# Kernel tuning notes

Measured on AMD Instinct MI355X. Metric: run time of the kernel, lower is better.

The kernel has to match this reference:

```python
import jax, jax.numpy as jnp
import numpy as np

N_NODES = 50000
N_EDGES = 800000
IN_DIM = 128
HID = 128
OUT_DIM = 64
NUM_GRAPHS = 512
GM_P = 2.0
EPS = 1e-6


def setup_inputs() -> dict:
    key = jax.random.key(0)
    ks = jax.random.split(key, 12)
    x = jax.random.normal(ks[0], (N_NODES, IN_DIM), dtype=jnp.float32)
    edge_index = jax.random.randint(ks[1], (2, N_EDGES), 0, N_NODES, dtype=jnp.int64)
    batch = jnp.sort(jax.random.randint(ks[2], (N_NODES,), 0, NUM_GRAPHS, dtype=jnp.int64))
    def lin(k, fan_in, fan_out):
        w = jax.random.normal(k, (fan_in, fan_out), dtype=jnp.float32) / np.sqrt(fan_in)
        return w
    return {
        "x": x,
        "edge_index": edge_index,
        "batch": batch,
        # 3 GCN conv layers (weight + bias each)
        "W0": lin(ks[3], IN_DIM, HID), "b0": jnp.zeros((HID,), jnp.float32),
        "W1": lin(ks[4], HID, HID),    "b1": jnp.zeros((HID,), jnp.float32),
        "W2": lin(ks[5], HID, HID),    "b2": jnp.zeros((HID,), jnp.float32),
        # 2 FF layers: [HID->HID], [HID->OUT_DIM]
        "Wf0": lin(ks[6], HID, HID),   "bf0": jnp.zeros((HID,), jnp.float32),
        "Wf1": lin(ks[7], HID, OUT_DIM), "bf1": jnp.zeros((OUT_DIM,), jnp.float32),
    }


def _gcn_layer(h, src, dst, deg_inv_sqrt, W, b):
    # PyG GCNConv: h' = D^-1/2 (A + I) D^-1/2 (h W) + b, deg includes self-loop
    h = h @ W                                           # [N, F]
    norm = deg_inv_sqrt[src] * deg_inv_sqrt[dst]        # [E]
    msg = h[src] * norm[:, None]                        # gather + scale, [E, F]
    agg = jax.ops.segment_sum(msg, dst, num_segments=N_NODES)
    agg = agg + h * (deg_inv_sqrt * deg_inv_sqrt)[:, None]   # self-loop term (norm = 1/deg)
    return agg + b


def _gm_pool(x, batch, p):
    # sign-preserving generalized mean pool via scatter_mean
    xt = jnp.sign(x) * (jnp.abs(x) + EPS) ** p
    sums = jax.ops.segment_sum(xt, batch, num_segments=NUM_GRAPHS)
    cnt = jax.ops.segment_sum(jnp.ones((x.shape[0],), x.dtype), batch, num_segments=NUM_GRAPHS)
    pooled = sums / jnp.maximum(cnt, 1.0)[:, None]
    return jnp.sign(pooled) * (jnp.abs(pooled) + EPS) ** (1.0 / p)


def reference(x, edge_index, batch, W0, b0, W1, b1, W2, b2, Wf0, bf0, Wf1, bf1):
    src, dst = edge_index[0], edge_index[1]
    # degree of aggregation targets, with +1 for self-loops (computed once; graph is static)
    deg = jax.ops.segment_sum(jnp.ones((N_EDGES,), x.dtype), dst, num_segments=N_NODES) + 1.0
    deg_inv_sqrt = jax.lax.rsqrt(deg)

    h = _gcn_layer(x, src, dst, deg_inv_sqrt, W0, b0)
    h = jax.nn.relu(h)
    h = _gcn_layer(h, src, dst, deg_inv_sqrt, W1, b1)
    h = jax.nn.relu(h)
    h = _gcn_layer(h, src, dst, deg_inv_sqrt, W2, b2)  # no relu after last conv

    graph_repr = _gm_pool(h, batch, GM_P)              # [G, HID]
    graph_repr = jax.nn.relu(graph_repr)

    z = jax.nn.relu(graph_repr @ Wf0 + bf0)
    logits = z @ Wf1 + bf1                             # [G, OUT_DIM]
    return logits
```

## Files before the change

### kernel.cpp

```cpp
#include <hip/hip_runtime.h>

#define N_NODES   50000
#define M_PAD     50048
#define N_TILES   1564
#define GEMM_GRID 782
#define N_EDGES   800000
#define HID       128
#define OUT_DIM   64
#define NUM_GRAPHS 512
#define EPS       1e-6f
#define NBUCK     196
#define BUCKCAP   6144
#define ABLOCKS   98

typedef __attribute__((ext_vector_type(8))) short short8;
typedef __attribute__((ext_vector_type(16))) float f32x16;

static __device__ __forceinline__ unsigned short f2bf(float f) {
    unsigned u = __builtin_bit_cast(unsigned, f);
    u += 0x7FFFu + ((u >> 16) & 1u);
    return (unsigned short)(u >> 16);
}
static __device__ __forceinline__ float bf2f(unsigned short h) {
    unsigned u = ((unsigned)h) << 16;
    return __builtin_bit_cast(float, u);
}
static __device__ __forceinline__ float lo16(unsigned w) {
    return __builtin_bit_cast(float, w << 16);
}
static __device__ __forceinline__ float hi16(unsigned w) {
    return __builtin_bit_cast(float, w & 0xFFFF0000u);
}

static __device__ __forceinline__ float signpow(float x, bool sqrt_mode) {
    if (x == 0.0f) return 0.0f;
    float a = fabsf(x) + EPS;
    float v = sqrt_mode ? sqrtf(a) : a * a;
    return x > 0.0f ? v : -v;
}

__global__ void k_wsplit3(const float* __restrict__ W0, const float* __restrict__ W1,
                          const float* __restrict__ W2, short* __restrict__ Wth,
                          short* __restrict__ Wtl, int* __restrict__ gcnt) {
    int which = blockIdx.y;
    if (which == 0 && blockIdx.x == 0 && threadIdx.x < NBUCK)
        gcnt[threadIdx.x] = 0;
    const float* W = which == 0 ? W0 : (which == 1 ? W1 : W2);
    int tid = blockIdx.x * blockDim.x + threadIdx.x;
    int k = tid & 127, n = tid >> 7;
    float w = W[k * HID + n];
    unsigned short h = f2bf(w);
    Wth[which * HID * HID + n * HID + k] = (short)h;
    Wtl[which * HID * HID + n * HID + k] = (short)f2bf(w - bf2f(h));
}

__global__ __launch_bounds__(256) void k_bucketize(const int* __restrict__ ei,
                                                   int* __restrict__ gcnt,
                                                   unsigned* __restrict__ ebuf) {
    __shared__ int lcnt[NBUCK];
    __shared__ int lbase[NBUCK];
    int tid = threadIdx.x;
    for (int i = tid; i < NBUCK; i += 256) lcnt[i] = 0;
    __syncthreads();

    const uint4* src4 = (const uint4*)ei;
    const uint4* dst4 = (const uint4*)(ei + N_EDGES);
    int base4 = blockIdx.x * 2048;

    #pragma unroll 1
    for (int it = 0; it < 8; it++) {
        int i4 = base4 + it * 256 + tid;
        if (i4 < N_EDGES / 4) {
            uint4 d = dst4[i4];
            atomicAdd(&lcnt[d.x >> 8], 1);
            atomicAdd(&lcnt[d.y >> 8], 1);
            atomicAdd(&lcnt[d.z >> 8], 1);
            atomicAdd(&lcnt[d.w >> 8], 1);
        }
    }
    __syncthreads();
    for (int i = tid; i < NBUCK; i += 256) {
        lbase[i] = atomicAdd(&gcnt[i], lcnt[i]);
        lcnt[i] = 0;
    }
    __syncthreads();

    #pragma unroll 1
    for (int it = 0; it < 8; it++) {
        int i4 = base4 + it * 256 + tid;
        if (i4 < N_EDGES / 4) {
            uint4 d = dst4[i4];
            uint4 s = src4[i4];
            unsigned dd[4] = {d.x, d.y, d.z, d.w};
            unsigned ss[4] = {s.x, s.y, s.z, s.w};
            #pragma unroll
            for (int k = 0; k < 4; k++) {
                int b = dd[k] >> 8;
                int p = atomicAdd(&lcnt[b], 1);
                ebuf[(size_t)b * BUCKCAP + lbase[b] + p] = ss[k] | (dd[k] << 16);
            }
        }
    }
}

__global__ __launch_bounds__(256) void k_csr(const unsigned* __restrict__ ebuf,
                                             const int* __restrict__ gcnt,
                                             int* __restrict__ offs,
                                             float* __restrict__ dis,
                                             int* __restrict__ csr) {
    __shared__ int cntA[256];
    __shared__ int scanA[256];
    __shared__ int sbase;
    int b = blockIdx.x;
    int t = threadIdx.x;
    int n0 = b * 256;

    int v = (t < NBUCK) ? gcnt[t] : 0;
    scanA[t] = v;
    __syncthreads();
    for (int off = 1; off < 256; off <<= 1) {
        int u = (t >= off) ? scanA[t - off] : 0;
        __syncthreads();
        scanA[t] += u;
        __syncthreads();
    }
    if (t == 0) sbase = (b == 0) ? 0 : scanA[b - 1];
    __syncthreads();
    int base  = sbase;
    int count = gcnt[b];
    const unsigned* eb = ebuf + (size_t)b * BUCKCAP;

    cntA[t] = 0;
    __syncthreads();
    for (int i = t; i < count; i += 256)
        atomicAdd(&cntA[eb[i] >> 16 & 0xFF], 1);
    __syncthreads();
    int c = cntA[t];
    scanA[t] = c;
    __syncthreads();
    for (int off = 1; off < 256; off <<= 1) {
        int u = (t >= off) ? scanA[t - off] : 0;
        __syncthreads();
        scanA[t] += u;
        __syncthreads();
    }
    int excl = scanA[t] - c;
    int n = n0 + t;
    if (n < N_NODES) {
        offs[n] = base + excl;
        dis[n]  = rsqrtf((float)c + 1.0f);
    }
    if (b == 0 && t == 0) offs[N_NODES] = N_EDGES;
    scanA[t] = excl;
    cntA[t] = 0;
    __syncthreads();
    for (int i = t; i < count; i += 256) {
        unsigned vv = eb[i];
        int ln = (vv >> 16) & 0xFF;
        int p = atomicAdd(&cntA[ln], 1);
        csr[base + scanA[ln] + p] = (int)(vv & 0xFFFFu);
    }
}

template<int FP32SRC>
__global__ __launch_bounds__(256) void k_gemm_mfma(const void* __restrict__ Asrc,
                                                   const short* __restrict__ Wh,
                                                   const short* __restrict__ Wl,
                                                   unsigned short* __restrict__ th,
                                                   const float* __restrict__ scale) {
    __shared__ short As_h[32 * 128];
    __shared__ short As_l[32 * 128];
    int tid  = threadIdx.x;
    int lane = tid & 63;
    int col  = (tid >> 6) * 32 + (lane & 31);
    int kh   = lane >> 5;
    int r    = lane & 31;

    short8 bh[8], bl[8];
    #pragma unroll
    for (int ks = 0; ks < 8; ks++) {
        bh[ks] = *(const short8*)(Wh + (size_t)col * HID + ks * 16 + kh * 8);
        bl[ks] = *(const short8*)(Wl + (size_t)col * HID + ks * 16 + kh * 8);
    }

    int su0 = tid, su1 = tid + 256;
    int sr0 = su0 >> 4, sc0 = su0 & 15;
    int sr1 = su1 >> 4, sc1 = su1 & 15;
    int sw0 = sr0 * 128 + ((sc0 ^ (sr0 & 7)) * 8);
    int sw1 = sr1 * 128 + ((sc1 ^ (sr1 & 7)) * 8);

    for (int tile = blockIdx.x; tile < N_TILES; tile += GEMM_GRID) {
        int row0 = tile * 32;
        __syncthreads();
        if (FP32SRC) {
            const float* gx = (const float*)Asrc;
            #pragma unroll
            for (int u = 0; u < 2; u++) {
                int sr = u ? sr1 : sr0, sc = u ? sc1 : sc0, sw = u ? sw1 : sw0;
                int gr = row0 + sr; if (gr >= N_NODES) gr = N_NODES - 1;
                const float* src = gx + (size_t)gr * HID + sc * 8;
                float4 a = ((const float4*)src)[0];
                float4 b = ((const float4*)src)[1];
                float vals[8] = {a.x, a.y, a.z, a.w, b.x, b.y, b.z, b.w};
                short8 hi, lo;
                #pragma unroll
                for (int j = 0; j < 8; j++) {
                    unsigned short hh = f2bf(vals[j]);
                    hi[j] = (short)hh;
                    lo[j] = (short)f2bf(vals[j] - bf2f(hh));
                }
                *(short8*)&As_h[sw] = hi;
                *(short8*)&As_l[sw] = lo;
            }
        } else {
            const short* gh = (const short*)Asrc + (size_t)row0 * HID;
            *(short8*)&As_h[sw0] = *(const short8*)(gh + sr0 * HID + sc0 * 8);
            *(short8*)&As_h[sw1] = *(const short8*)(gh + sr1 * HID + sc1 * 8);
        }
        __syncthreads();

        f32x16 acc = {0.f};
        if (FP32SRC) {
            short8 ah[8], al[8];
            #pragma unroll
            for (int ks = 0; ks < 8; ks++) {
                int cg = ks * 2 + kh;
                int off = r * 128 + ((cg ^ (r & 7)) * 8);
                ah[ks] = *(const short8*)&As_h[off];
                al[ks] = *(const short8*)&As_l[off];
            }
            #pragma unroll
            for (int ks = 0; ks < 8; ks++) {
                acc = __builtin_amdgcn_mfma_f32_32x32x16_bf16(ah[ks], bh[ks], acc, 0, 0, 0);
                acc = __builtin_amdgcn_mfma_f32_32x32x16_bf16(al[ks], bh[ks], acc, 0, 0, 0);
                acc = __builtin_amdgcn_mfma_f32_32x32x16_bf16(ah[ks], bl[ks], acc, 0, 0, 0);
            }
        } else {
            short8 ah[8];
            #pragma unroll
            for (int ks = 0; ks < 8; ks++) {
                int cg = ks * 2 + kh;
                int off = r * 128 + ((cg ^ (r & 7)) * 8);
                ah[ks] = *(const short8*)&As_h[off];
            }
            #pragma unroll
            for (int ks = 0; ks < 8; ks++) {
                acc = __builtin_amdgcn_mfma_f32_32x32x16_bf16(ah[ks], bh[ks], acc, 0, 0, 0);
                acc = __builtin_amdgcn_mfma_f32_32x32x16_bf16(ah[ks], bl[ks], acc, 0, 0, 0);
            }
        }

        #pragma unroll
        for (int reg = 0; reg < 16; reg++) {
            int row = row0 + (reg & 3) + 8 * (reg >> 2) + 4 * kh;
            float v = acc[reg] * scale[row];
            th[(size_t)row * HID + col] = f2bf(v);
        }
    }
}

__global__ __launch_bounds__(256) void k_agg(const unsigned short* __restrict__ th,
                                             const int* __restrict__ offs,
                                             const int* __restrict__ csr_src,
                                             const float* __restrict__ dis,
                                             const float* __restrict__ bias,
                                             float* __restrict__ hout,
                                             short* __restrict__ hh,
                                             int mode) {
    int node = blockIdx.x * 4 + (threadIdx.x >> 6);
    if (node >= N_NODES) return;
    int lane = threadIdx.x & 63;
    int c  = lane & 15;
    int e  = lane >> 4;
    int beg = offs[node], end = offs[node + 1];
    float dn = dis[node];

    float a[8] = {};
    for (int j = beg; j < end; j += 8) {
        #pragma unroll
        for (int k = 0; k < 2; k++) {
            int jj = j + k * 4 + e;
            int jc = jj < end ? jj : end - 1;
            int s = csr_src[jc];
            float m = (jj < end) ? 1.0f : 0.0f;
            uint4 v = *(const uint4*)&th[(size_t)s * HID + c * 8];
            a[0] = fmaf(lo16(v.x), m, a[0]);
            a[1] = fmaf(hi16(v.x), m, a[1]);
            a[2] = fmaf(lo16(v.y), m, a[2]);
            a[3] = fmaf(hi16(v.y), m, a[3]);
            a[4] = fmaf(lo16(v.z), m, a[4]);
            a[5] = fmaf(hi16(v.z), m, a[5]);
            a[6] = fmaf(lo16(v.w), m, a[6]);
            a[7] = fmaf(hi16(v.w), m, a[7]);
        }
    }
    #pragma unroll
    for (int i = 0; i < 8; i++) {
        a[i] += __shfl_xor(a[i], 16);
        a[i] += __shfl_xor(a[i], 32);
    }

    if (e == 0) {
        uint4 sh = *(const uint4*)&th[(size_t)node * HID + c * 8];
        float4 b0 = *(const float4*)&bias[c * 8];
        float4 b1 = *(const float4*)&bias[c * 8 + 4];
        float o[8];
        o[0] = (a[0] + lo16(sh.x)) * dn + b0.x;
        o[1] = (a[1] + hi16(sh.x)) * dn + b0.y;
        o[2] = (a[2] + lo16(sh.y)) * dn + b0.z;
        o[3] = (a[3] + hi16(sh.y)) * dn + b0.w;
        o[4] = (a[4] + lo16(sh.z)) * dn + b1.x;
        o[5] = (a[5] + hi16(sh.z)) * dn + b1.y;
        o[6] = (a[6] + lo16(sh.w)) * dn + b1.z;
        o[7] = (a[7] + hi16(sh.w)) * dn + b1.w;
        if (mode == 1) {
            ushort4 vh0, vh1;
            #pragma unroll
            for (int i = 0; i < 8; i++) o[i] = fmaxf(o[i], 0.f);
            vh0.x = f2bf(o[0]); vh0.y = f2bf(o[1]); vh0.z = f2bf(o[2]); vh0.w = f2bf(o[3]);
            vh1.x = f2bf(o[4]); vh1.y = f2bf(o[5]); vh1.z = f2bf(o[6]); vh1.w = f2bf(o[7]);
            *(ushort4*)&hh[(size_t)node * HID + c * 8]     = vh0;
            *(ushort4*)&hh[(size_t)node * HID + c * 8 + 4] = vh1;
        } else {
            float4 o0 = make_float4(o[0], o[1], o[2], o[3]);
            float4 o1 = make_float4(o[4], o[5], o[6], o[7]);
            *(float4*)&hout[(size_t)node * HID + c * 8]     = o0;
            *(float4*)&hout[(size_t)node * HID + c * 8 + 4] = o1;
        }
    }
}

__global__ __launch_bounds__(256) void k_poolff(const float* __restrict__ h,
                                                const int* __restrict__ batch,
                                                const float* __restrict__ Wf0,
                                                const float* __restrict__ bf0,
                                                const float* __restrict__ Wf1,
                                                const float* __restrict__ bf1,
                                                float* __restrict__ out) {
    __shared__ float smx[4][64], smy[4][64];
    __shared__ float row[128], zrow[128];
    __shared__ int bnd[2];
    int g = blockIdx.x;
    int t = threadIdx.x;
    if (t < 2) {
        int target = g + t;
        int lo = 0, hi = N_NODES;
        while (lo < hi) {
            int mid = (lo + hi) >> 1;
            if (batch[mid] < target) lo = mid + 1; else hi = mid;
        }
        bnd[t] = lo;
    }
    __syncthreads();
    int beg = bnd[0], end = bnd[1];

    int c = t & 63, slot = t >> 6;
    float sx = 0.f, sy = 0.f;
    for (int n = beg + slot; n < end; n += 4) {
        float2 v = *(const float2*)&h[(size_t)n * HID + c * 2];
        sx += signpow(v.x, false);
        sy += signpow(v.y, false);
    }
    smx[slot][c] = sx; smy[slot][c] = sy;
    __syncthreads();
    if (slot == 0) {
        sx = (smx[0][c] + smx[1][c]) + (smx[2][c] + smx[3][c]);
        sy = (smy[0][c] + smy[1][c]) + (smy[2][c] + smy[3][c]);
        float cnt = fmaxf((float)(end - beg), 1.0f);
        row[c * 2]     = fmaxf(signpow(sx / cnt, true), 0.f);
        row[c * 2 + 1] = fmaxf(signpow(sy / cnt, true), 0.f);
    }
    __syncthreads();
    if (t < 128) {
        float acc = bf0[t];
        #pragma unroll 8
        for (int k = 0; k < 128; k++) acc = fmaf(row[k], Wf0[k * 128 + t], acc);
        zrow[t] = fmaxf(acc, 0.f);
    }
    __syncthreads();
    if (t < OUT_DIM) {
        float a2 = bf1[t];
        #pragma unroll 8
        for (int k = 0; k < 128; k++) a2 = fmaf(zrow[k], Wf1[k * OUT_DIM + t], a2);
        out[g * OUT_DIM + t] = a2;
    }
}

static inline size_t align256(size_t x) { return (x + 255) & ~(size_t)255; }

extern "C" void kernel_launch(void* const* d_in, const int* in_sizes, int n_in,
                              void* d_out, int out_size, void* d_ws, size_t ws_size,
                              hipStream_t stream) {
    const float* x     = (const float*)d_in[0];
    const int*   ei    = (const int*)d_in[1];
    const int*   batch = (const int*)d_in[2];
    const float* W0  = (const float*)d_in[3];  const float* b0  = (const float*)d_in[4];
    const float* W1  = (const float*)d_in[5];  const float* b1  = (const float*)d_in[6];
    const float* W2  = (const float*)d_in[7];  const float* b2  = (const float*)d_in[8];
    const float* Wf0 = (const float*)d_in[9];  const float* bf0 = (const float*)d_in[10];
    const float* Wf1 = (const float*)d_in[11]; const float* bf1 = (const float*)d_in[12];
    float* out = (float*)d_out;

    char* p = (char*)d_ws;
    unsigned short* th = (unsigned short*)p; p += align256((size_t)M_PAD * HID * 2);
    short* hA    = (short*)p; p += align256((size_t)M_PAD * HID * 2);
    short* hB    = (short*)p; p += align256((size_t)M_PAD * HID * 2);
    float* h     = (float*)p; p += align256((size_t)M_PAD * HID * 4);
    unsigned* ebuf = (unsigned*)p; p += align256((size_t)NBUCK * BUCKCAP * 4);
    int*   gcnt    = (int*)p;   p += align256((size_t)NBUCK * 4);
    int*   offs    = (int*)p;   p += align256((size_t)(N_NODES + 1) * 4);
    int*   csr     = (int*)p;   p += align256((size_t)N_EDGES * 4);
    float* dis     = (float*)p; p += align256((size_t)N_NODES * 4);
    short* Wth     = (short*)p; p += align256((size_t)3 * HID * HID * 2);
    short* Wtl     = (short*)p; p += align256((size_t)3 * HID * HID * 2);

    dim3 wg(64, 3);
    k_wsplit3<<<wg, 256, 0, stream>>>(W0, W1, W2, Wth, Wtl, gcnt);
    k_bucketize<<<ABLOCKS, 256, 0, stream>>>(ei, gcnt, ebuf);
    k_csr      <<<NBUCK, 256, 0, stream>>>(ebuf, gcnt, offs, dis, csr);

    int agg_blocks = (N_NODES + 3) / 4;

    k_gemm_mfma<1><<<GEMM_GRID, 256, 0, stream>>>(x, Wth, Wtl, th, dis);
    k_agg<<<agg_blocks, 256, 0, stream>>>(th, offs, csr, dis, b0, nullptr, hB, 1);
    k_gemm_mfma<0><<<GEMM_GRID, 256, 0, stream>>>(hB, Wth + HID * HID, Wtl + HID * HID, th, dis);
    k_agg<<<agg_blocks, 256, 0, stream>>>(th, offs, csr, dis, b1, nullptr, hA, 1);
    k_gemm_mfma<0><<<GEMM_GRID, 256, 0, stream>>>(hA, Wth + 2 * HID * HID, Wtl + 2 * HID * HID, th, dis);
    k_agg<<<agg_blocks, 256, 0, stream>>>(th, offs, csr, dis, b2, h, nullptr, 0);

    k_poolff<<<NUM_GRAPHS, 256, 0, stream>>>(h, batch, Wf0, bf0, Wf1, bf1, out);
}
```

Before: 203.2 us.

## Prefetch next GEMM tile into registers and store final conv output as bf16

The GEMM kernel now issues global loads for the next 32-row tile while the current tile is converted, staged in LDS and run through MFMA, so load latency can overlap with compute. The last aggregation layer now writes bf16 instead of fp32, and the pooling kernel reads bf16. This halves that layer's write traffic and the pooling read traffic, at the cost of bf16 rounding before the generalized-mean pooling. Each GEMM block covers only two tiles (782 blocks over 1564 tiles), so the prefetch hides latency on just one iteration, and it keeps more registers live.

```diff
diff --git a/kernel.cpp b/kernel.cpp
--- a/kernel.cpp
+++ b/kernel.cpp
@@ -183,39 +183,66 @@
         bl[ks] = *(const short8*)(Wl + (size_t)col * HID + ks * 16 + kh * 8);
     }
 
-    int su0 = tid, su1 = tid + 256;
-    int sr0 = su0 >> 4, sc0 = su0 & 15;
-    int sr1 = su1 >> 4, sc1 = su1 & 15;
+    int sr0 = tid >> 4,          sc0 = tid & 15;
+    int sr1 = (tid + 256) >> 4,  sc1 = (tid + 256) & 15;
     int sw0 = sr0 * 128 + ((sc0 ^ (sr0 & 7)) * 8);
     int sw1 = sr1 * 128 + ((sc1 ^ (sr1 & 7)) * 8);
 
-    for (int tile = blockIdx.x; tile < N_TILES; tile += GEMM_GRID) {
-        int row0 = tile * 32;
-        __syncthreads();
+    float4 pa0_, pb0_, pa1_, pb1_;
+    short8 ph0_, ph1_;
+
+    {
+        int row0 = blockIdx.x * 32;
         if (FP32SRC) {
             const float* gx = (const float*)Asrc;
-            #pragma unroll
-            for (int u = 0; u < 2; u++) {
-                int sr = u ? sr1 : sr0, sc = u ? sc1 : sc0, sw = u ? sw1 : sw0;
-                int gr = row0 + sr; if (gr >= N_NODES) gr = N_NODES - 1;
-                const float* src = gx + (size_t)gr * HID + sc * 8;
-                float4 a = ((const float4*)src)[0];
-                float4 b = ((const float4*)src)[1];
-                float vals[8] = {a.x, a.y, a.z, a.w, b.x, b.y, b.z, b.w};
-                short8 hi, lo;
-                #pragma unroll
-                for (int j = 0; j < 8; j++) {
-                    unsigned short hh = f2bf(vals[j]);
-                    hi[j] = (short)hh;
-                    lo[j] = (short)f2bf(vals[j] - bf2f(hh));
-                }
-                *(short8*)&As_h[sw] = hi;
-                *(short8*)&As_l[sw] = lo;
-            }
+            int g0 = row0 + sr0; if (g0 >= N_NODES) g0 = N_NODES - 1;
+            int g1 = row0 + sr1; if (g1 >= N_NODES) g1 = N_NODES - 1;
+            const float* s0 = gx + (size_t)g0 * HID + sc0 * 8;
+            const float* s1 = gx + (size_t)g1 * HID + sc1 * 8;
+            pa0_ = ((const float4*)s0)[0]; pb0_ = ((const float4*)s0)[1];
+            pa1_ = ((const float4*)s1)[0]; pb1_ = ((const float4*)s1)[1];
         } else {
             const short* gh = (const short*)Asrc + (size_t)row0 * HID;
-            *(short8*)&As_h[sw0] = *(const short8*)(gh + sr0 * HID + sc0 * 8);
-            *(short8*)&As_h[sw1] = *(const short8*)(gh + sr1 * HID + sc1 * 8);
+            ph0_ = *(const short8*)(gh + sr0 * HID + sc0 * 8);
+            ph1_ = *(const short8*)(gh + sr1 * HID + sc1 * 8);
+        }
+    }
+
+    for (int tile = blockIdx.x; tile < N_TILES; tile += GEMM_GRID) {
+        __syncthreads();
+        if (FP32SRC) {
+            float v0[8] = {pa0_.x, pa0_.y, pa0_.z, pa0_.w, pb0_.x, pb0_.y, pb0_.z, pb0_.w};
+            float v1[8] = {pa1_.x, pa1_.y, pa1_.z, pa1_.w, pb1_.x, pb1_.y, pb1_.z, pb1_.w};
+            short8 h0, l0, h1, l1;
+            #pragma unroll
+            for (int j = 0; j < 8; j++) {
+                unsigned short hh0 = f2bf(v0[j]);
+                h0[j] = (short)hh0; l0[j] = (short)f2bf(v0[j] - bf2f(hh0));
+                unsigned short hh1 = f2bf(v1[j]);
+                h1[j] = (short)hh1; l1[j] = (short)f2bf(v1[j] - bf2f(hh1));
+            }
+            *(short8*)&As_h[sw0] = h0; *(short8*)&As_l[sw0] = l0;
+            *(short8*)&As_h[sw1] = h1; *(short8*)&As_l[sw1] = l1;
+        } else {
+            *(short8*)&As_h[sw0] = ph0_;
+            *(short8*)&As_h[sw1] = ph1_;
+        }
+        int nt = tile + GEMM_GRID;
+        if (nt < N_TILES) {
+            int row0 = nt * 32;
+            if (FP32SRC) {
+                const float* gx = (const float*)Asrc;
+                int g0 = row0 + sr0; if (g0 >= N_NODES) g0 = N_NODES - 1;
+                int g1 = row0 + sr1; if (g1 >= N_NODES) g1 = N_NODES - 1;
+                const float* s0 = gx + (size_t)g0 * HID + sc0 * 8;
+                const float* s1 = gx + (size_t)g1 * HID + sc1 * 8;
+                pa0_ = ((const float4*)s0)[0]; pb0_ = ((const float4*)s0)[1];
+                pa1_ = ((const float4*)s1)[0]; pb1_ = ((const float4*)s1)[1];
+            } else {
+                const short* gh = (const short*)Asrc + (size_t)row0 * HID;
+                ph0_ = *(const short8*)(gh + sr0 * HID + sc0 * 8);
+                ph1_ = *(const short8*)(gh + sr1 * HID + sc1 * 8);
+            }
         }
         __syncthreads();
 
@@ -250,6 +277,7 @@
             }
         }
 
+        int row0 = tile * 32;
         #pragma unroll
         for (int reg = 0; reg < 16; reg++) {
             int row = row0 + (reg & 3) + 8 * (reg >> 2) + 4 * kh;
@@ -264,9 +292,8 @@
                                              const int* __restrict__ csr_src,
                                              const float* __restrict__ dis,
                                              const float* __restrict__ bias,
-                                             float* __restrict__ hout,
                                              short* __restrict__ hh,
-                                             int mode) {
+                                             int relu) {
     int node = blockIdx.x * 4 + (threadIdx.x >> 6);
     if (node >= N_NODES) return;
     int lane = threadIdx.x & 63;
@@ -313,24 +340,19 @@
         o[5] = (a[5] + hi16(sh.z)) * dn + b1.y;
         o[6] = (a[6] + lo16(sh.w)) * dn + b1.z;
         o[7] = (a[7] + hi16(sh.w)) * dn + b1.w;
-        if (mode == 1) {
-            ushort4 vh0, vh1;
+        if (relu) {
             #pragma unroll
             for (int i = 0; i < 8; i++) o[i] = fmaxf(o[i], 0.f);
-            vh0.x = f2bf(o[0]); vh0.y = f2bf(o[1]); vh0.z = f2bf(o[2]); vh0.w = f2bf(o[3]);
-            vh1.x = f2bf(o[4]); vh1.y = f2bf(o[5]); vh1.z = f2bf(o[6]); vh1.w = f2bf(o[7]);
-            *(ushort4*)&hh[(size_t)node * HID + c * 8]     = vh0;
-            *(ushort4*)&hh[(size_t)node * HID + c * 8 + 4] = vh1;
-        } else {
-            float4 o0 = make_float4(o[0], o[1], o[2], o[3]);
-            float4 o1 = make_float4(o[4], o[5], o[6], o[7]);
-            *(float4*)&hout[(size_t)node * HID + c * 8]     = o0;
-            *(float4*)&hout[(size_t)node * HID + c * 8 + 4] = o1;
-        }
-    }
-}
-
-__global__ __launch_bounds__(256) void k_poolff(const float* __restrict__ h,
+        }
+        ushort4 vh0, vh1;
+        vh0.x = f2bf(o[0]); vh0.y = f2bf(o[1]); vh0.z = f2bf(o[2]); vh0.w = f2bf(o[3]);
+        vh1.x = f2bf(o[4]); vh1.y = f2bf(o[5]); vh1.z = f2bf(o[6]); vh1.w = f2bf(o[7]);
+        *(ushort4*)&hh[(size_t)node * HID + c * 8]     = vh0;
+        *(ushort4*)&hh[(size_t)node * HID + c * 8 + 4] = vh1;
+    }
+}
+
+__global__ __launch_bounds__(256) void k_poolff(const unsigned short* __restrict__ h,
                                                 const int* __restrict__ batch,
                                                 const float* __restrict__ Wf0,
                                                 const float* __restrict__ bf0,
@@ -357,9 +379,9 @@
     int c = t & 63, slot = t >> 6;
     float sx = 0.f, sy = 0.f;
     for (int n = beg + slot; n < end; n += 4) {
-        float2 v = *(const float2*)&h[(size_t)n * HID + c * 2];
-        sx += signpow(v.x, false);
-        sy += signpow(v.y, false);
+        unsigned w = *(const unsigned*)&h[(size_t)n * HID + c * 2];
+        sx += signpow(lo16(w), false);
+        sy += signpow(hi16(w), false);
     }
     smx[slot][c] = sx; smy[slot][c] = sy;
     __syncthreads();
@@ -405,7 +427,6 @@
     unsigned short* th = (unsigned short*)p; p += align256((size_t)M_PAD * HID * 2);
     short* hA    = (short*)p; p += align256((size_t)M_PAD * HID * 2);
     short* hB    = (short*)p; p += align256((size_t)M_PAD * HID * 2);
-    float* h     = (float*)p; p += align256((size_t)M_PAD * HID * 4);
     unsigned* ebuf = (unsigned*)p; p += align256((size_t)NBUCK * BUCKCAP * 4);
     int*   gcnt    = (int*)p;   p += align256((size_t)NBUCK * 4);
     int*   offs    = (int*)p;   p += align256((size_t)(N_NODES + 1) * 4);
@@ -422,11 +443,11 @@
     int agg_blocks = (N_NODES + 3) / 4;
 
     k_gemm_mfma<1><<<GEMM_GRID, 256, 0, stream>>>(x, Wth, Wtl, th, dis);
-    k_agg<<<agg_blocks, 256, 0, stream>>>(th, offs, csr, dis, b0, nullptr, hB, 1);
+    k_agg<<<agg_blocks, 256, 0, stream>>>(th, offs, csr, dis, b0, hB, 1);
     k_gemm_mfma<0><<<GEMM_GRID, 256, 0, stream>>>(hB, Wth + HID * HID, Wtl + HID * HID, th, dis);
-    k_agg<<<agg_blocks, 256, 0, stream>>>(th, offs, csr, dis, b1, nullptr, hA, 1);
+    k_agg<<<agg_blocks, 256, 0, stream>>>(th, offs, csr, dis, b1, hA, 1);
     k_gemm_mfma<0><<<GEMM_GRID, 256, 0, stream>>>(hA, Wth + 2 * HID * HID, Wtl + 2 * HID * HID, th, dis);
-    k_agg<<<agg_blocks, 256, 0, stream>>>(th, offs, csr, dis, b2, h, nullptr, 0);
-
-    k_poolff<<<NUM_GRAPHS, 256, 0, stream>>>(h, batch, Wf0, bf0, Wf1, bf1, out);
-}
+    k_agg<<<agg_blocks, 256, 0, stream>>>(th, offs, csr, dis, b2, hB, 0);
+
+    k_poolff<<<NUM_GRAPHS, 256, 0, stream>>>((const unsigned short*)hB, batch, Wf0, bf0, Wf1, bf1, out);
+}
```

After: 203.8 us. No clear change (+0.3%).
